# Optimization experiments

Hardware: AMD Instinct MI355X
Metric: run time of the kernel (lower is better)

The kernel has to match this reference:

```python
import jax, jax.numpy as jnp
import numpy as np

N_NODES = 50000
N_EDGES = 1600000
KSIZE = 5   # kernel_size per dim
DIM = 3     # pseudo-coordinate dim


def spline_conv(x, src, dst, pseudo, W, root, bias, num_nodes):
    # Open B-spline basis, degree 1 (PyG SplineConv defaults).
    pos = pseudo * (KSIZE - 1)                         # [E, 3]
    idx = jnp.clip(jnp.floor(pos), 0, KSIZE - 2).astype(jnp.int32)
    frac = pos - idx                                   # [E, 3]
    strides = jnp.array([1, KSIZE, KSIZE * KSIZE], dtype=jnp.int32)
    x_j = x[src]                                       # [E, in]
    msg = jnp.zeros((src.shape[0], W.shape[-1]), x.dtype)
    # 2^dim = 8 active basis combinations per edge (small fixed loop).
    for b in range(2 ** DIM):
        bits = np.array([(b >> d) & 1 for d in range(DIM)])
        kidx = ((idx + jnp.asarray(bits, jnp.int32)) * strides).sum(-1)   # [E]
        basis = jnp.prod(jnp.where(jnp.asarray(bits, bool), frac, 1.0 - frac), axis=-1)  # [E]
        msg = msg + basis[:, None] * jnp.einsum('ei,eio->eo', x_j, W[kidx])
    out = jax.ops.segment_sum(msg, dst, num_segments=num_nodes)
    return out + x @ root + bias


def setup_inputs() -> dict:
    key = jax.random.key(0)
    ks = jax.random.split(key, 8)
    x = jax.random.normal(ks[0], (N_NODES, 1), jnp.float32)
    edge_index = jax.random.randint(ks[1], (2, N_EDGES), 0, N_NODES, jnp.int64)
    pseudo = jax.random.uniform(ks[2], (N_EDGES, DIM), jnp.float32)
    K = KSIZE ** DIM
    W1 = jax.random.normal(ks[3], (K, 1, 8), jnp.float32) * 0.1
    root1 = jax.random.normal(ks[4], (1, 8), jnp.float32) * 0.1
    bias1 = jnp.zeros((8,), jnp.float32)
    W2 = jax.random.normal(ks[5], (K, 8, 1), jnp.float32) * 0.1
    root2 = jax.random.normal(ks[6], (8, 1), jnp.float32) * 0.1
    bias2 = jnp.zeros((1,), jnp.float32)
    return {"x": x, "edge_index": edge_index, "pseudo": pseudo,
            "W1": W1, "root1": root1, "bias1": bias1,
            "W2": W2, "root2": root2, "bias2": bias2}


def reference(x, edge_index, pseudo, W1, root1, bias1, W2, root2, bias2):
    src = edge_index[0]
    dst = edge_index[1]
    n = x.shape[0]
    h = jax.nn.elu(spline_conv(x, src, dst, pseudo, W1, root1, bias1, n))
    out = jax.nn.elu(spline_conv(h, src, dst, pseudo, W2, root2, bias2, n))
    return out.reshape(-1)
```

## Files before the change

kernel.cpp:

```cpp
#include <hip/hip_runtime.h>
#include <math.h>

#define NK    125
#define HID   8
#define BSH   6
#define BKT   64
#define CAP   2560
#define MAXNB 1024
#define NBLK  512
#define WS    12

__device__ __forceinline__ float eluf(float v) {
    return v > 0.f ? v : expf(v) - 1.f;
}


__global__ __launch_bounds__(256) void init_cursor(int* __restrict__ cursor, int NB) {
    int b = blockIdx.x * 256 + threadIdx.x;
    if (b < NB) cursor[b] = b * CAP;
}

__global__ __launch_bounds__(256) void partition_edges(
    const int* __restrict__ src, const int* __restrict__ dst,
    const float* __restrict__ pseudo,
    int* __restrict__ cursor, int4* __restrict__ payload,
    int E, int NB, int chunk)
{
    __shared__ int lcnt[MAXNB];
    __shared__ int lbase[MAXNB];
    int e0 = blockIdx.x * chunk;
    int e1 = min(e0 + chunk, E);

    for (int b = threadIdx.x; b < NB; b += 256) lcnt[b] = 0;
    __syncthreads();

    for (int e = e0 + threadIdx.x; e < e1; e += 256)
        atomicAdd(&lcnt[dst[e] >> BSH], 1);
    __syncthreads();

    for (int b = threadIdx.x; b < NB; b += 256) {
        int c = lcnt[b];
        lbase[b] = c ? atomicAdd(&cursor[b], c) : 0;
        lcnt[b] = 0;
    }
    __syncthreads();

    for (int e = e0 + threadIdx.x; e < e1; e += 256) {
        int d = dst[e];
        int b = d >> BSH;
        int off = atomicAdd(&lcnt[b], 1);
        int pos = lbase[b] + off;
        if (pos < (b + 1) * CAP) {
            float p0 = pseudo[3 * e + 0] * 4.f;
            float p1 = pseudo[3 * e + 1] * 4.f;
            float p2 = pseudo[3 * e + 2] * 4.f;
            int i0 = min(max((int)floorf(p0), 0), 3);
            int i1 = min(max((int)floorf(p1), 0), 3);
            int i2 = min(max((int)floorf(p2), 0), 3);
            float f0 = p0 - (float)i0, f1 = p1 - (float)i1, f2 = p2 - (float)i2;
            int kb = i0 + 5 * i1 + 25 * i2;
            int packed = src[e] | (kb << 16) | ((d & (BKT - 1)) << 23);
            payload[pos] = make_int4(packed, __float_as_int(f0),
                                     __float_as_int(f1), __float_as_int(f2));
        }
    }
}

__global__ __launch_bounds__(512) void layer1_fused(
    int4* __restrict__ payload, const int* __restrict__ cursor,
    const float* __restrict__ x, const float* __restrict__ W1,
    const float* __restrict__ root1, const float* __restrict__ bias1,
    float* __restrict__ h, int* __restrict__ ns, int* __restrict__ ne, int N)
{
    __shared__ float sW[NK * WS];
    __shared__ int4 stage[CAP];
    __shared__ unsigned short perm[CAP];
    __shared__ int hist[BKT];
    __shared__ int off[BKT + 1];
    __shared__ int cur[BKT];

    for (int i = threadIdx.x; i < NK * HID; i += 512)
        sW[(i >> 3) * WS + (i & 7)] = W1[i];
    if (threadIdx.x < BKT) hist[threadIdx.x] = 0;
    __syncthreads();

    int bkt  = blockIdx.x;
    int base = bkt * CAP;
    int cnt  = min(cursor[bkt] - base, CAP);

    for (int i = threadIdx.x; i < cnt; i += 512) {
        int4 pl = payload[base + i];
        stage[i] = pl;
        atomicAdd(&hist[(pl.x >> 23) & (BKT - 1)], 1);
    }
    __syncthreads();

    if (threadIdx.x < BKT) {
        int v = hist[threadIdx.x];
        int incl = v;
        for (int d = 1; d < BKT; d <<= 1) {
            int u = __shfl_up(incl, d, 64);
            if (threadIdx.x >= d) incl += u;
        }
        off[threadIdx.x + 1] = incl;
        if (threadIdx.x == 0) off[0] = 0;
        cur[threadIdx.x] = incl - v;
    }
    __syncthreads();

    for (int i = threadIdx.x; i < cnt; i += 512) {
        int nl = (stage[i].x >> 23) & (BKT - 1);
        int pos = atomicAdd(&cur[nl], 1);
        perm[pos] = (unsigned short)i;
    }
    __syncthreads();

    for (int i = threadIdx.x; i < cnt; i += 512)
        payload[base + i] = stage[perm[i]];
    if (threadIdx.x < BKT) {
        int n = (bkt << BSH) + threadIdx.x;
        if (n < N) {
            ns[n] = base + off[threadIdx.x];
            ne[n] = base + off[threadIdx.x + 1];
        }
    }

    int nl = threadIdx.x >> 3;
    int j  = threadIdx.x & 7;
    int s = off[nl], e = off[nl + 1];

    float4 aclo = make_float4(0.f, 0.f, 0.f, 0.f);
    float4 achi = make_float4(0.f, 0.f, 0.f, 0.f);

    for (int i = s + j; i < e; i += 8) {
        int4 pl = stage[perm[i]];
        int packed = pl.x;
        float f0 = __int_as_float(pl.y);
        float f1 = __int_as_float(pl.z);
        float f2 = __int_as_float(pl.w);
        int sidx = packed & 0xFFFF;
        int kb   = (packed >> 16) & 0x7F;
        float xj = x[sidx];
#pragma unroll
        for (int b = 0; b < 8; ++b) {
            int kidx = kb + (b & 1) + ((b >> 1) & 1) * 5 + ((b >> 2) & 1) * 25;
            float basis = ((b & 1) ? f0 : 1.f - f0)
                        * ((b & 2) ? f1 : 1.f - f1)
                        * ((b & 4) ? f2 : 1.f - f2);
            float w = xj * basis;
            float4 wlo = *(const float4*)&sW[kidx * WS];
            float4 whi = *(const float4*)&sW[kidx * WS + 4];
            aclo.x += w * wlo.x; aclo.y += w * wlo.y;
            aclo.z += w * wlo.z; aclo.w += w * wlo.w;
            achi.x += w * whi.x; achi.y += w * whi.y;
            achi.z += w * whi.z; achi.w += w * whi.w;
        }
    }

    float acc[HID] = {aclo.x, aclo.y, aclo.z, aclo.w, achi.x, achi.y, achi.z, achi.w};
#pragma unroll
    for (int m = 1; m < 8; m <<= 1)
#pragma unroll
        for (int o = 0; o < HID; ++o)
            acc[o] += __shfl_xor(acc[o], m, 64);

    int n = (bkt << BSH) + nl;
    if (n < N) {
        float v = acc[j] + x[n] * root1[j] + bias1[j];
        h[(size_t)n * HID + j] = eluf(v);
    }
}

__global__ __launch_bounds__(256) void layer2_csr(
    const int4* __restrict__ payload, const int* __restrict__ ns,
    const int* __restrict__ ne, const float* __restrict__ h,
    const float* __restrict__ W2, const float* __restrict__ root2,
    const float* __restrict__ bias2, float* __restrict__ out, int N)
{
    __shared__ float sW[NK * WS];
    for (int i = threadIdx.x; i < NK * HID; i += 256)
        sW[(i >> 3) * WS + (i & 7)] = W2[i];
    __syncthreads();

    int n = blockIdx.x * 32 + (threadIdx.x >> 3);
    int j = threadIdx.x & 7;
    int s = 0, e = 0;
    if (n < N) { s = ns[n]; e = ne[n]; }

    float msg = 0.f;
    for (int i = s + j; i < e; i += 8) {
        int4 pl = payload[i];
        int packed = pl.x;
        float f0 = __int_as_float(pl.y);
        float f1 = __int_as_float(pl.z);
        float f2 = __int_as_float(pl.w);
        int sidx = packed & 0xFFFF;
        int kb   = (packed >> 16) & 0x7F;
        const float4* hp = (const float4*)(h + (size_t)sidx * HID);
        float4 ha = hp[0];
        float4 hb = hp[1];
#pragma unroll
        for (int b = 0; b < 8; ++b) {
            int kidx = kb + (b & 1) + ((b >> 1) & 1) * 5 + ((b >> 2) & 1) * 25;
            float basis = ((b & 1) ? f0 : 1.f - f0)
                        * ((b & 2) ? f1 : 1.f - f1)
                        * ((b & 4) ? f2 : 1.f - f2);
            float4 wlo = *(const float4*)&sW[kidx * WS];
            float4 whi = *(const float4*)&sW[kidx * WS + 4];
            float dot = ha.x * wlo.x + ha.y * wlo.y + ha.z * wlo.z + ha.w * wlo.w
                      + hb.x * whi.x + hb.y * whi.y + hb.z * whi.z + hb.w * whi.w;
            msg += basis * dot;
        }
    }

    if (n < N) msg += h[(size_t)n * HID + j] * root2[j];

#pragma unroll
    for (int m = 1; m < 8; m <<= 1)
        msg += __shfl_xor(msg, m, 64);

    if (j == 0 && n < N)
        out[n] = eluf(msg + bias2[0]);
}


__global__ __launch_bounds__(256) void spline_edge1(
    const int* __restrict__ src, const int* __restrict__ dst,
    const float* __restrict__ pseudo, const float* __restrict__ x,
    const float* __restrict__ W1, float* __restrict__ hacc, int E)
{
    __shared__ float sW[HID * NK];
    for (int i = threadIdx.x; i < HID * NK; i += blockDim.x) {
        int k = i >> 3, o = i & 7;
        sW[o * NK + k] = W1[i];
    }
    __syncthreads();
    int e = blockIdx.x * blockDim.x + threadIdx.x;
    if (e >= E) return;
    float p0 = pseudo[3 * e + 0] * 4.f, p1 = pseudo[3 * e + 1] * 4.f, p2 = pseudo[3 * e + 2] * 4.f;
    int i0 = min(max((int)floorf(p0), 0), 3);
    int i1 = min(max((int)floorf(p1), 0), 3);
    int i2 = min(max((int)floorf(p2), 0), 3);
    float f0 = p0 - i0, f1 = p1 - i1, f2 = p2 - i2;
    int kbase = i0 + 5 * i1 + 25 * i2;
    float xj = x[src[e]];
    float acc[HID];
#pragma unroll
    for (int o = 0; o < HID; ++o) acc[o] = 0.f;
#pragma unroll
    for (int b = 0; b < 8; ++b) {
        int kidx = kbase + (b & 1) + ((b >> 1) & 1) * 5 + ((b >> 2) & 1) * 25;
        float basis = ((b & 1) ? f0 : 1.f - f0) * ((b & 2) ? f1 : 1.f - f1) * ((b & 4) ? f2 : 1.f - f2);
#pragma unroll
        for (int o = 0; o < HID; ++o) acc[o] += basis * sW[o * NK + kidx];
    }
    float* hp = hacc + (size_t)dst[e] * HID;
#pragma unroll
    for (int o = 0; o < HID; ++o) atomicAdd(hp + o, xj * acc[o]);
}

__global__ __launch_bounds__(256) void node1(
    float* __restrict__ h, const float* __restrict__ x,
    const float* __restrict__ root1, const float* __restrict__ bias1, int N)
{
    int t = blockIdx.x * blockDim.x + threadIdx.x;
    if (t >= N * HID) return;
    int n = t >> 3, o = t & 7;
    h[t] = eluf(h[t] + x[n] * root1[o] + bias1[o]);
}

__global__ __launch_bounds__(256) void spline_edge2(
    const int* __restrict__ src, const int* __restrict__ dst,
    const float* __restrict__ pseudo, const float* __restrict__ h,
    const float* __restrict__ W2, float* __restrict__ oacc, int E)
{
    __shared__ float sW[HID * NK];
    for (int idx = threadIdx.x; idx < HID * NK; idx += blockDim.x) {
        int k = idx >> 3, i = idx & 7;
        sW[i * NK + k] = W2[idx];
    }
    __syncthreads();
    int e = blockIdx.x * blockDim.x + threadIdx.x;
    if (e >= E) return;
    float p0 = pseudo[3 * e + 0] * 4.f, p1 = pseudo[3 * e + 1] * 4.f, p2 = pseudo[3 * e + 2] * 4.f;
    int i0 = min(max((int)floorf(p0), 0), 3);
    int i1 = min(max((int)floorf(p1), 0), 3);
    int i2 = min(max((int)floorf(p2), 0), 3);
    float f0 = p0 - i0, f1 = p1 - i1, f2 = p2 - i2;
    int kbase = i0 + 5 * i1 + 25 * i2;
    const float4* hp4 = (const float4*)(h + (size_t)src[e] * HID);
    float4 ha = hp4[0], hb = hp4[1];
    float hj[HID] = {ha.x, ha.y, ha.z, ha.w, hb.x, hb.y, hb.z, hb.w};
    float msg = 0.f;
#pragma unroll
    for (int b = 0; b < 8; ++b) {
        int kidx = kbase + (b & 1) + ((b >> 1) & 1) * 5 + ((b >> 2) & 1) * 25;
        float basis = ((b & 1) ? f0 : 1.f - f0) * ((b & 2) ? f1 : 1.f - f1) * ((b & 4) ? f2 : 1.f - f2);
        float dot = 0.f;
#pragma unroll
        for (int i = 0; i < HID; ++i) dot += hj[i] * sW[i * NK + kidx];
        msg += basis * dot;
    }
    atomicAdd(&oacc[dst[e]], msg);
}

__global__ __launch_bounds__(256) void node2(
    const float* __restrict__ oacc, const float* __restrict__ h,
    const float* __restrict__ root2, const float* __restrict__ bias2,
    float* __restrict__ out, int N)
{
    int n = blockIdx.x * blockDim.x + threadIdx.x;
    if (n >= N) return;
    float v = oacc[n] + bias2[0];
#pragma unroll
    for (int i = 0; i < HID; ++i) v += h[(size_t)n * HID + i] * root2[i];
    out[n] = eluf(v);
}


extern "C" void kernel_launch(void* const* d_in, const int* in_sizes, int n_in,
                              void* d_out, int out_size, void* d_ws, size_t ws_size,
                              hipStream_t stream) {
    const float* x      = (const float*)d_in[0];
    const int*   ei     = (const int*)d_in[1];
    const float* pseudo = (const float*)d_in[2];
    const float* W1     = (const float*)d_in[3];
    const float* root1  = (const float*)d_in[4];
    const float* bias1  = (const float*)d_in[5];
    const float* W2     = (const float*)d_in[6];
    const float* root2  = (const float*)d_in[7];
    const float* bias2  = (const float*)d_in[8];

    int N = in_sizes[0];
    int E = in_sizes[1] / 2;
    const int* src = ei;
    const int* dst = ei + E;

    int NB = (N + BKT - 1) >> BSH;
    size_t payload_bytes = (size_t)NB * CAP * sizeof(int4);
    size_t h_bytes       = (size_t)N * HID * sizeof(float);
    size_t cursor_bytes  = (size_t)NB * sizeof(int);
    size_t nsne_bytes    = (size_t)N * sizeof(int);
    size_t need = payload_bytes + h_bytes + cursor_bytes + 2 * nsne_bytes + 64;

    if (NB <= MAXNB && N <= 65536 && ws_size >= need) {
        char* p = (char*)d_ws;
        int4*  payload = (int4*)p;                 p += payload_bytes;
        float* h       = (float*)p;                p += h_bytes;
        int*   cursor  = (int*)p;                  p += cursor_bytes;
        int*   ns      = (int*)p;                  p += nsne_bytes;
        int*   ne      = (int*)p;

        init_cursor<<<(NB + 255) / 256, 256, 0, stream>>>(cursor, NB);
        int chunk = (E + NBLK - 1) / NBLK;
        partition_edges<<<NBLK, 256, 0, stream>>>(src, dst, pseudo, cursor, payload, E, NB, chunk);
        layer1_fused<<<NB, 512, 0, stream>>>(payload, cursor, x, W1, root1, bias1, h, ns, ne, N);
        layer2_csr<<<(N + 31) / 32, 256, 0, stream>>>(payload, ns, ne, h, W2, root2, bias2, (float*)d_out, N);
    } else {
        float* h    = (float*)d_ws;
        float* oacc = h + (size_t)N * HID;
        hipMemsetAsync(d_ws, 0, (size_t)(N * HID + N) * sizeof(float), stream);
        int eg = (E + 255) / 256;
        spline_edge1<<<eg, 256, 0, stream>>>(src, dst, pseudo, x, W1, h, E);
        node1<<<(N * HID + 255) / 256, 256, 0, stream>>>(h, x, root1, bias1, N);
        spline_edge2<<<eg, 256, 0, stream>>>(src, dst, pseudo, h, W2, oacc, E);
        node2<<<(N + 255) / 256, 256, 0, stream>>>(oacc, h, root2, bias2, (float*)d_out, N);
    }
}
```

Before: 172.4 us.

## Stage partitioned edges in LDS and write payload coalesced by bucket

```diff
diff --git a/kernel.cpp b/kernel.cpp
--- a/kernel.cpp
+++ b/kernel.cpp
@@ -7,7 +7,7 @@
 #define BKT   64
 #define CAP   2560
 #define MAXNB 1024
-#define NBLK  512
+#define CHUNK 2816
 #define WS    12
 
 __device__ __forceinline__ float eluf(float v) {
@@ -24,45 +24,74 @@
     const int* __restrict__ src, const int* __restrict__ dst,
     const float* __restrict__ pseudo,
     int* __restrict__ cursor, int4* __restrict__ payload,
-    int E, int NB, int chunk)
-{
-    __shared__ int lcnt[MAXNB];
-    __shared__ int lbase[MAXNB];
-    int e0 = blockIdx.x * chunk;
-    int e1 = min(e0 + chunk, E);
-
-    for (int b = threadIdx.x; b < NB; b += 256) lcnt[b] = 0;
-    __syncthreads();
-
-    for (int e = e0 + threadIdx.x; e < e1; e += 256)
-        atomicAdd(&lcnt[dst[e] >> BSH], 1);
+    int E, int NB)
+{
+    __shared__ int4 stage[CHUNK];
+    __shared__ unsigned short perm[CHUNK];
+    __shared__ unsigned short sb[CHUNK];
+    __shared__ int s_off[MAXNB + 1];
+    __shared__ int s_gmo[MAXNB];
+
+    int e0  = blockIdx.x * CHUNK;
+    int cnt = min(CHUNK, E - e0);
+
+    for (int b = threadIdx.x; b < NB; b += 256) s_off[b] = 0;
+    __syncthreads();
+
+    for (int i = threadIdx.x; i < cnt; i += 256) {
+        int e = e0 + i;
+        int d = dst[e];
+        float p0 = pseudo[3 * e + 0] * 4.f;
+        float p1 = pseudo[3 * e + 1] * 4.f;
+        float p2 = pseudo[3 * e + 2] * 4.f;
+        int i0 = min(max((int)floorf(p0), 0), 3);
+        int i1 = min(max((int)floorf(p1), 0), 3);
+        int i2 = min(max((int)floorf(p2), 0), 3);
+        float f0 = p0 - (float)i0, f1 = p1 - (float)i1, f2 = p2 - (float)i2;
+        int kb = i0 + 5 * i1 + 25 * i2;
+        int packed = src[e] | (kb << 16) | ((d & (BKT - 1)) << 23);
+        stage[i] = make_int4(packed, __float_as_int(f0),
+                             __float_as_int(f1), __float_as_int(f2));
+        atomicAdd(&s_off[d >> BSH], 1);
+    }
+    __syncthreads();
+
+    if (threadIdx.x < 64) {
+        int per = (NB + 63) >> 6;
+        int lo = threadIdx.x * per, hi = min(lo + per, NB);
+        int sum = 0;
+        for (int b = lo; b < hi; ++b) { int v = s_off[b]; s_off[b] = sum; sum += v; }
+        int incl = sum;
+        for (int d2 = 1; d2 < 64; d2 <<= 1) {
+            int u = __shfl_up(incl, d2, 64);
+            if ((int)threadIdx.x >= d2) incl += u;
+        }
+        int basep = incl - sum;
+        for (int b = lo; b < hi; ++b) s_off[b] += basep;
+        if (threadIdx.x == 63) s_off[NB] = incl;
+    }
     __syncthreads();
 
     for (int b = threadIdx.x; b < NB; b += 256) {
-        int c = lcnt[b];
-        lbase[b] = c ? atomicAdd(&cursor[b], c) : 0;
-        lcnt[b] = 0;
-    }
-    __syncthreads();
-
-    for (int e = e0 + threadIdx.x; e < e1; e += 256) {
-        int d = dst[e];
-        int b = d >> BSH;
-        int off = atomicAdd(&lcnt[b], 1);
-        int pos = lbase[b] + off;
-        if (pos < (b + 1) * CAP) {
-            float p0 = pseudo[3 * e + 0] * 4.f;
-            float p1 = pseudo[3 * e + 1] * 4.f;
-            float p2 = pseudo[3 * e + 2] * 4.f;
-            int i0 = min(max((int)floorf(p0), 0), 3);
-            int i1 = min(max((int)floorf(p1), 0), 3);
-            int i2 = min(max((int)floorf(p2), 0), 3);
-            float f0 = p0 - (float)i0, f1 = p1 - (float)i1, f2 = p2 - (float)i2;
-            int kb = i0 + 5 * i1 + 25 * i2;
-            int packed = src[e] | (kb << 16) | ((d & (BKT - 1)) << 23);
-            payload[pos] = make_int4(packed, __float_as_int(f0),
-                                     __float_as_int(f1), __float_as_int(f2));
-        }
+        int c = s_off[b + 1] - s_off[b];
+        int g = c ? atomicAdd(&cursor[b], c) : 0;
+        s_gmo[b] = g - s_off[b];
+    }
+    __syncthreads();
+
+    for (int i = threadIdx.x; i < cnt; i += 256) {
+        int b = dst[e0 + i] >> BSH;
+        int r = atomicAdd(&s_off[b], 1);
+        perm[r] = (unsigned short)i;
+        sb[r]   = (unsigned short)b;
+    }
+    __syncthreads();
+
+    for (int o = threadIdx.x; o < cnt; o += 256) {
+        int b = sb[o];
+        int g = s_gmo[b] + o;
+        if (g < (b + 1) * CAP)
+            payload[g] = stage[perm[o]];
     }
 }
 
@@ -352,8 +381,8 @@
         int*   ne      = (int*)p;
 
         init_cursor<<<(NB + 255) / 256, 256, 0, stream>>>(cursor, NB);
-        int chunk = (E + NBLK - 1) / NBLK;
-        partition_edges<<<NBLK, 256, 0, stream>>>(src, dst, pseudo, cursor, payload, E, NB, chunk);
+        int pblocks = (E + CHUNK - 1) / CHUNK;
+        partition_edges<<<pblocks, 256, 0, stream>>>(src, dst, pseudo, cursor, payload, E, NB);
         layer1_fused<<<NB, 512, 0, stream>>>(payload, cursor, x, W1, root1, bias1, h, ns, ne, N);
         layer2_csr<<<(N + 31) / 32, 256, 0, stream>>>(payload, ns, ne, h, W2, root2, bias2, (float*)d_out, N);
     } else {
```

Measured after the change: 167.9 us. 1.03x faster.
